# Performance work log

Hardware: AMD Instinct MI355X
Metric: run time of the kernel (lower is better)

## Reference

```python
import jax, jax.numpy as jnp
import numpy as np

D = 256
H = 4
HD = D // H


def setup_inputs() -> dict:
    key = jax.random.key(0)
    ks = jax.random.split(key, 12)
    A, T = 64, 512
    s = 1.0 / np.sqrt(D)
    return {
        "features": jax.random.normal(ks[0], (A, T, D), jnp.float32),
        "positions": jax.random.normal(ks[1], (A, T, 2), jnp.float32),
        "Wq": jax.random.normal(ks[2], (D, D), jnp.float32) * s,
        "bq": jnp.zeros((D,), jnp.float32),
        "Wk": jax.random.normal(ks[3], (D, D), jnp.float32) * s,
        "bk": jnp.zeros((D,), jnp.float32),
        "Wv": jax.random.normal(ks[4], (D, D), jnp.float32) * s,
        "bv": jnp.zeros((D,), jnp.float32),
        "Wo": jax.random.normal(ks[5], (D, D), jnp.float32) * s,
        "bo": jnp.zeros((D,), jnp.float32),
        "max_distance": 2,
        "time_window": 64,
    }


def _sparse_mask(positions, max_distance, time_window):
    # positions: [A, T, 2] -> allowed [A, T, T]
    A, T, _ = positions.shape
    diff = positions[:, :, None, :] - positions[:, None, :, :]  # [A,T,T,2]
    dist2 = jnp.sum(diff * diff, axis=-1)                       # [A,T,T]
    t = jnp.arange(T)
    tmask = jnp.abs(t[:, None] - t[None, :]) <= time_window      # [T,T]
    return (dist2 <= float(max_distance) ** 2) & tmask[None]     # [A,T,T]


def reference(features, positions, Wq, bq, Wk, bk, Wv, bv, Wo, bo,
              max_distance, time_window):
    A, T, Dm = features.shape
    allowed = _sparse_mask(positions, max_distance, time_window)  # [A,T,T]
    q = features @ Wq.T + bq
    k = features @ Wk.T + bk
    v = features @ Wv.T + bv
    # split heads: [A, T, H, HD]
    q = q.reshape(A, T, H, HD)
    k = k.reshape(A, T, H, HD)
    v = v.reshape(A, T, H, HD)
    scale = 1.0 / np.sqrt(HD)
    scores = jnp.einsum("athd,ashd->ahts", q, k) * scale          # [A,H,T,T]
    scores = jnp.where(allowed[:, None], scores, -jnp.inf)
    attn = jax.nn.softmax(scores, axis=-1)
    out = jnp.einsum("ahts,ashd->athd", attn, v).reshape(A, T, Dm)
    return out @ Wo.T + bo
```

## Files before the change

kernel.cpp:

```cpp
#include <hip/hip_runtime.h>
#include <hip/hip_bf16.h>
#include <cstdint>
#include <cstddef>

typedef __attribute__((ext_vector_type(8))) _Float16 half8;
typedef __attribute__((ext_vector_type(4))) float floatx4;

#define MFMA16(a, b, c) __builtin_amdgcn_mfma_f32_16x16x32_f16((a), (b), (c), 0, 0, 0)

#define GLOAD_LDS16(g, l)                                                     \
    __builtin_amdgcn_global_load_lds(                                         \
        (const __attribute__((address_space(1))) void*)(g),                   \
        (__attribute__((address_space(3))) void*)(l), 16, 0, 0)

#define NFEAT 8388608

__device__ __forceinline__ void stage_dma(
    const _Float16* __restrict__ src, _Float16* __restrict__ lds,
    int wid, int lane)
{
#pragma unroll
    for (int i = 0; i < 4; ++i) {
        int grp = wid * 4 + i;
        int row = grp * 8 + (lane >> 3);
        int sc  = (lane & 7) ^ (row & 7);
        GLOAD_LDS16(src + (size_t)row * 256 + sc * 8, lds + grp * 512);
    }
}

__device__ __forceinline__ void stage_f32_s(
    const float* __restrict__ src, _Float16* __restrict__ lds, int tid,
    int dst_stride)
{
#pragma unroll
    for (int i = 0; i < 4; ++i) {
        int g   = tid + 256 * i;
        int row = g >> 3, chd = g & 7;
        int chs = chd ^ (row & 7);
        const float* s = src + (size_t)row * 256 + chs * 8;
        float4 v0 = *(const float4*)s;
        float4 v1 = *(const float4*)(s + 4);
        half8 h = { (_Float16)v0.x, (_Float16)v0.y, (_Float16)v0.z, (_Float16)v0.w,
                    (_Float16)v1.x, (_Float16)v1.y, (_Float16)v1.z, (_Float16)v1.w };
        *(half8*)(&lds[row * dst_stride + chd * 8]) = h;
    }
}

__global__ __launch_bounds__(256) void qkv_fused(
    const float* __restrict__ feat,
    const float* __restrict__ Wq, const float* __restrict__ Wk,
    const float* __restrict__ Wv,
    const float* __restrict__ bq, const float* __restrict__ bk,
    const float* __restrict__ bv,
    _Float16* __restrict__ Qb, _Float16* __restrict__ Kb, _Float16* __restrict__ Vb)
{
    __shared__ _Float16 Xs[128 * 256];
    __shared__ _Float16 Ws[128 * 64];

    const int n   = blockIdx.x;
    const int idx = n >> 3;
    const int bm  = (n & 7) * 32 + (idx >> 1);
    const int bn  = idx & 1;

    const int tid  = threadIdx.x;
    const int lane = tid & 63, wid = tid >> 6;
    const int quad = lane >> 4, l16 = lane & 15;
    const int wm = wid & 1, wn = wid >> 1;

    const float* Xg = feat + (size_t)bm * 128 * 256;
#pragma unroll
    for (int slab = 0; slab < 4; ++slab)
        stage_f32_s(Xg + slab * 64, Xs + slab * 64, tid, 256);
    __syncthreads();

#pragma unroll 1
    for (int z = 0; z < 3; ++z) {
        const float* W    = (z == 0) ? Wq : (z == 1) ? Wk : Wv;
        const float* bias = (z == 0) ? bq : (z == 1) ? bk : bv;
        _Float16*    outp = (z == 0) ? Qb : (z == 1) ? Kb : Vb;
        const float* Wg = W + (size_t)bn * 128 * 256;

        floatx4 acc[4][4] = {};
#pragma unroll 1
        for (int ks = 0; ks < 4; ++ks) {
            stage_f32_s(Wg + ks * 64, Ws, tid, 64);
            __syncthreads();
#pragma unroll
            for (int kh = 0; kh < 2; ++kh) {
                half8 af[4], bf[4];
#pragma unroll
                for (int mi = 0; mi < 4; ++mi) {
                    int row = wm * 64 + mi * 16 + l16;
                    int cs  = (kh * 4 + quad) ^ (row & 7);
                    af[mi] = *(const half8*)(&Xs[row * 256 + ks * 64 + cs * 8]);
                }
#pragma unroll
                for (int ni = 0; ni < 4; ++ni) {
                    int row = wn * 64 + ni * 16 + l16;
                    int cs  = (kh * 4 + quad) ^ (row & 7);
                    bf[ni] = *(const half8*)(&Ws[row * 64 + cs * 8]);
                }
#pragma unroll
                for (int mi = 0; mi < 4; ++mi)
#pragma unroll
                    for (int ni = 0; ni < 4; ++ni)
                        acc[mi][ni] = MFMA16(af[mi], bf[ni], acc[mi][ni]);
            }
            __syncthreads();
        }

#pragma unroll
        for (int ni = 0; ni < 4; ++ni) {
            int col = bn * 128 + wn * 64 + ni * 16 + l16;
            float bv2 = bias[col];
#pragma unroll
            for (int mi = 0; mi < 4; ++mi)
#pragma unroll
                for (int r = 0; r < 4; ++r) {
                    int row = bm * 128 + wm * 64 + mi * 16 + quad * 4 + r;
                    outp[(size_t)row * 256 + col] = (_Float16)(acc[mi][ni][r] + bv2);
                }
        }
    }
}

__global__ __launch_bounds__(256) void out_gemm(
    const _Float16* __restrict__ attnH, const float* __restrict__ Wo,
    const float* __restrict__ bo, float* __restrict__ out)
{
    __shared__ _Float16 As[128 * 64];
    __shared__ _Float16 Bs[128 * 64];

    const int n   = blockIdx.x;
    const int idx = n >> 3;
    const int bm  = (n & 7) * 32 + (idx >> 1);
    const int bn  = idx & 1;

    const int tid  = threadIdx.x;
    const int lane = tid & 63, wid = tid >> 6;
    const int quad = lane >> 4, l16 = lane & 15;
    const int wm = wid & 1, wn = wid >> 1;

    floatx4 acc[4][4] = {};
    const float* Wg = Wo + (size_t)bn * 128 * 256;

    for (int k0 = 0; k0 < 256; k0 += 64) {
        stage_dma(attnH + (size_t)bm * 128 * 256 + k0, As, wid, lane);
        stage_f32_s(Wg + k0, Bs, tid, 64);
        __syncthreads();
#pragma unroll
        for (int kh = 0; kh < 2; ++kh) {
            half8 af[4], bf[4];
#pragma unroll
            for (int mi = 0; mi < 4; ++mi) {
                int row = wm * 64 + mi * 16 + l16;
                int cs  = (kh * 4 + quad) ^ (row & 7);
                af[mi] = *(const half8*)(&As[row * 64 + cs * 8]);
            }
#pragma unroll
            for (int ni = 0; ni < 4; ++ni) {
                int row = wn * 64 + ni * 16 + l16;
                int cs  = (kh * 4 + quad) ^ (row & 7);
                bf[ni] = *(const half8*)(&Bs[row * 64 + cs * 8]);
            }
#pragma unroll
            for (int mi = 0; mi < 4; ++mi)
#pragma unroll
                for (int ni = 0; ni < 4; ++ni)
                    acc[mi][ni] = MFMA16(af[mi], bf[ni], acc[mi][ni]);
        }
        __syncthreads();
    }

#pragma unroll
    for (int ni = 0; ni < 4; ++ni) {
        int col = bn * 128 + wn * 64 + ni * 16 + l16;
        float bv = bo[col];
#pragma unroll
        for (int mi = 0; mi < 4; ++mi)
#pragma unroll
            for (int r = 0; r < 4; ++r) {
                int row = bm * 128 + wm * 64 + mi * 16 + quad * 4 + r;
                out[(size_t)row * 256 + col] = acc[mi][ni][r] + bv;
            }
    }
}

__global__ __launch_bounds__(256) void attn_kernel(
    const _Float16* __restrict__ Qb, const _Float16* __restrict__ Kb,
    const _Float16* __restrict__ Vb, const float* __restrict__ positions,
    const int* __restrict__ mdp, const int* __restrict__ twp,
    _Float16* __restrict__ attnb)
{
    const int n   = blockIdx.x;
    const int idx = n >> 3;
    const int a   = (n & 7) * 8 + (idx >> 5);
    const int rem = idx & 31;
    const int qt  = rem >> 2, h = rem & 3;

    const int q0 = qt * 64;
    const int s_base = q0 - 64;
    const int tid = threadIdx.x, lane = tid & 63, wid = tid >> 6;
    const int quad = lane >> 4, l16 = lane & 15;

    __shared__ _Float16 KPs[192 * 64];
    __shared__ _Float16 Vt[64 * 192];

    const size_t abase = (size_t)a * 512;
    const int md = *mdp, tw = *twp;
    const float md2 = (float)(md * md);

    const size_t qrow = abase + q0 + wid * 16 + l16;
    half8 aq0 = *(const half8*)(Qb + qrow * 256 + h * 64 + quad * 8);
    half8 aq1 = *(const half8*)(Qb + qrow * 256 + h * 64 + 32 + quad * 8);
    float qpx[4], qpy[4];
    int trow[4];
#pragma unroll
    for (int r = 0; r < 4; ++r) {
        int m = wid * 16 + quad * 4 + r;
        trow[r] = q0 + m;
        float2 qp = *(const float2*)(positions + (abase + q0 + m) * 2);
        qpx[r] = qp.x;
        qpy[r] = qp.y;
    }

#pragma unroll
    for (int i = 0; i < 6; ++i) {
        int grp = wid * 6 + i;
        int si  = grp * 8 + (lane >> 3);
        int sc  = min(max(s_base + si, 0), 511);
        int ch  = (lane & 7) ^ (si & 7);
        GLOAD_LDS16(Kb + (abase + sc) * 256 + h * 64 + ch * 8, KPs + grp * 512);
    }
#pragma unroll
    for (int i = 0; i < 3; ++i) {
        int g   = tid + 256 * i;
        int si2 = (g % 96) * 2;
        int d0  = (g / 96) * 8;
        int sa  = min(max(s_base + si2, 0), 511);
        int sb  = min(max(s_base + si2 + 1, 0), 511);
        half8 v0 = *(const half8*)(Vb + (abase + sa) * 256 + h * 64 + d0);
        half8 v1 = *(const half8*)(Vb + (abase + sb) * 256 + h * 64 + d0);
        int c = si2 >> 3;
#pragma unroll
        for (int j = 0; j < 8; ++j) {
            int d  = d0 + j;
            int cs = (c & ~7) | ((c & 7) ^ (d & 7));
            union { _Float16 hh[2]; uint32_t u; } p;
            p.hh[0] = v0[j]; p.hh[1] = v1[j];
            *(uint32_t*)(&Vt[d * 192 + cs * 8 + (si2 & 7)]) = p.u;
        }
    }
    __syncthreads();

    floatx4 S[12];
#pragma unroll
    for (int j = 0; j < 12; ++j) {
        int si = j * 16 + l16;
        half8 bk0 = *(const half8*)(&KPs[si * 64 + ((quad) ^ (si & 7)) * 8]);
        half8 bk1 = *(const half8*)(&KPs[si * 64 + ((4 + quad) ^ (si & 7)) * 8]);
        floatx4 acc = {};
        acc = MFMA16(aq0, bk0, acc);
        acc = MFMA16(aq1, bk1, acc);
        int sr = s_base + si;
        int sc = min(max(sr, 0), 511);
        float2 kp = *(const float2*)(positions + (abase + sc) * 2);
        bool svalid = (sr >= 0) && (sr < 512);
#pragma unroll
        for (int r = 0; r < 4; ++r) {
            float dx = qpx[r] - kp.x, dy = qpy[r] - kp.y;
            float d2 = dx * dx + dy * dy;
            int dt = trow[r] - sr; dt = dt < 0 ? -dt : dt;
            bool ok = svalid && (d2 <= md2) && (dt <= tw);
            S[j][r] = ok ? acc[r] * 0.125f : -1e30f;
        }
    }

    float minv[4];
#pragma unroll
    for (int r = 0; r < 4; ++r) {
        float m = -1e30f;
#pragma unroll
        for (int j = 0; j < 12; ++j) m = fmaxf(m, S[j][r]);
        m = fmaxf(m, __shfl_xor(m, 1));
        m = fmaxf(m, __shfl_xor(m, 2));
        m = fmaxf(m, __shfl_xor(m, 4));
        m = fmaxf(m, __shfl_xor(m, 8));
        float l = 0.f;
#pragma unroll
        for (int j = 0; j < 12; ++j) {
            float p = __expf(S[j][r] - m);
            S[j][r] = p;
            l += p;
        }
        l += __shfl_xor(l, 1);
        l += __shfl_xor(l, 2);
        l += __shfl_xor(l, 4);
        l += __shfl_xor(l, 8);
        minv[r] = 1.0f / l;
    }

    __syncthreads();

    _Float16* Ps = KPs + wid * (16 * 192);
#pragma unroll
    for (int j = 0; j < 12; ++j)
#pragma unroll
        for (int r = 0; r < 4; ++r) {
            int row = quad * 4 + r;
            int col = j * 16 + l16;
            int ch  = (col >> 3) ^ (row & 7);
            Ps[row * 192 + ch * 8 + (col & 7)] = (_Float16)(S[j][r] * minv[r]);
        }

    half8 af[6];
#pragma unroll
    for (int k = 0; k < 6; ++k) {
        int ch = (k * 4 + quad) ^ (l16 & 7);
        af[k] = *(const half8*)(&Ps[l16 * 192 + ch * 8]);
    }
#pragma unroll
    for (int nn = 0; nn < 4; ++nn) {
        floatx4 accO = {};
#pragma unroll
        for (int k = 0; k < 6; ++k) {
            int row = nn * 16 + l16;
            int c   = k * 4 + quad;
            int cs  = (c & ~7) | ((c & 7) ^ (row & 7));
            half8 bv = *(const half8*)(&Vt[row * 192 + cs * 8]);
            accO = MFMA16(af[k], bv, accO);
        }
#pragma unroll
        for (int r = 0; r < 4; ++r) {
            int row = q0 + wid * 16 + quad * 4 + r;
            attnb[(abase + row) * 256 + h * 64 + nn * 16 + l16] = (_Float16)accO[r];
        }
    }
}

extern "C" void kernel_launch(void* const* d_in, const int* in_sizes, int n_in,
                              void* d_out, int out_size, void* d_ws, size_t ws_size,
                              hipStream_t stream)
{
    const float* feat = (const float*)d_in[0];
    const float* pos  = (const float*)d_in[1];
    const float* Wq   = (const float*)d_in[2];
    const float* bq   = (const float*)d_in[3];
    const float* Wk   = (const float*)d_in[4];
    const float* bk   = (const float*)d_in[5];
    const float* Wv   = (const float*)d_in[6];
    const float* bv   = (const float*)d_in[7];
    const float* Wo   = (const float*)d_in[8];
    const float* bo   = (const float*)d_in[9];
    const int*   md   = (const int*)d_in[10];
    const int*   tw   = (const int*)d_in[11];
    float*       out  = (float*)d_out;

    _Float16* ws    = (_Float16*)d_ws;
    _Float16* Qb    = ws;
    _Float16* Kb    = Qb + NFEAT;
    _Float16* Vb    = Kb + NFEAT;
    _Float16* attnH = Vb + NFEAT;

    qkv_fused<<<512, 256, 0, stream>>>(feat, Wq, Wk, Wv, bq, bk, bv, Qb, Kb, Vb);

    attn_kernel<<<2048, 256, 0, stream>>>(Qb, Kb, Vb, pos, md, tw, attnH);

    out_gemm<<<512, 256, 0, stream>>>(attnH, Wo, bo, out);
}
```

Measured before the change: 166.2 us.

## Prefetch weight tiles into registers and preload attention tile in projection GEMMs

In both the QKV projection and output projection GEMMs, the next fp32 weight k-slab is loaded into registers while the current slab is consumed. It is converted to fp16 and written to LDS at the start of the next step, replacing the previous synchronous stage-then-barrier loop. The QKV kernel also prefetches the first slab of the next weight matrix across z iterations. The output GEMM now DMA-loads the whole 128x256 attention tile into LDS up front instead of per k-step. The aim is to hide global load latency behind MFMA work, at the cost of more registers, more LDS and hand-written barrier/waitcnt asm.

```diff
diff --git a/kernel.cpp b/kernel.cpp
--- a/kernel.cpp
+++ b/kernel.cpp
@@ -13,20 +13,9 @@
         (const __attribute__((address_space(1))) void*)(g),                   \
         (__attribute__((address_space(3))) void*)(l), 16, 0, 0)
 
+#define BARLG() asm volatile("s_waitcnt lgkmcnt(0)\ns_barrier" ::: "memory")
+
 #define NFEAT 8388608
-
-__device__ __forceinline__ void stage_dma(
-    const _Float16* __restrict__ src, _Float16* __restrict__ lds,
-    int wid, int lane)
-{
-#pragma unroll
-    for (int i = 0; i < 4; ++i) {
-        int grp = wid * 4 + i;
-        int row = grp * 8 + (lane >> 3);
-        int sc  = (lane & 7) ^ (row & 7);
-        GLOAD_LDS16(src + (size_t)row * 256 + sc * 8, lds + grp * 512);
-    }
-}
 
 __device__ __forceinline__ void stage_f32_s(
     const float* __restrict__ src, _Float16* __restrict__ lds, int tid,
@@ -71,20 +60,49 @@
 #pragma unroll
     for (int slab = 0; slab < 4; ++slab)
         stage_f32_s(Xg + slab * 64, Xs + slab * 64, tid, 256);
+
+    float4 wv0[4], wv1[4];
+    auto loadw = [&](const float* __restrict__ src) {
+#pragma unroll
+        for (int i = 0; i < 4; ++i) {
+            int g = tid + 256 * i, row = g >> 3, chd = g & 7;
+            int chs = chd ^ (row & 7);
+            const float* s = src + (size_t)row * 256 + chs * 8;
+            wv0[i] = *(const float4*)s;
+            wv1[i] = *(const float4*)(s + 4);
+        }
+    };
+    auto writew = [&]() {
+#pragma unroll
+        for (int i = 0; i < 4; ++i) {
+            int g = tid + 256 * i, row = g >> 3, chd = g & 7;
+            half8 h = { (_Float16)wv0[i].x, (_Float16)wv0[i].y,
+                        (_Float16)wv0[i].z, (_Float16)wv0[i].w,
+                        (_Float16)wv1[i].x, (_Float16)wv1[i].y,
+                        (_Float16)wv1[i].z, (_Float16)wv1[i].w };
+            *(half8*)(&Ws[row * 64 + chd * 8]) = h;
+        }
+    };
+
+    const size_t boff = (size_t)bn * 128 * 256;
+    loadw(Wq + boff);
     __syncthreads();
 
 #pragma unroll 1
     for (int z = 0; z < 3; ++z) {
-        const float* W    = (z == 0) ? Wq : (z == 1) ? Wk : Wv;
+        const float* Wz   = (z == 0) ? Wq : (z == 1) ? Wk : Wv;
+        const float* Wnz  = (z == 0) ? Wk : Wv;
         const float* bias = (z == 0) ? bq : (z == 1) ? bk : bv;
         _Float16*    outp = (z == 0) ? Qb : (z == 1) ? Kb : Vb;
-        const float* Wg = W + (size_t)bn * 128 * 256;
 
         floatx4 acc[4][4] = {};
-#pragma unroll 1
+#pragma unroll
         for (int ks = 0; ks < 4; ++ks) {
-            stage_f32_s(Wg + ks * 64, Ws, tid, 64);
-            __syncthreads();
+            BARLG();
+            writew();
+            if (ks < 3)      loadw(Wz + boff + (ks + 1) * 64);
+            else if (z < 2)  loadw(Wnz + boff);
+            BARLG();
 #pragma unroll
             for (int kh = 0; kh < 2; ++kh) {
                 half8 af[4], bf[4];
@@ -106,7 +124,6 @@
                     for (int ni = 0; ni < 4; ++ni)
                         acc[mi][ni] = MFMA16(af[mi], bf[ni], acc[mi][ni]);
             }
-            __syncthreads();
         }
 
 #pragma unroll
@@ -128,7 +145,7 @@
     const _Float16* __restrict__ attnH, const float* __restrict__ Wo,
     const float* __restrict__ bo, float* __restrict__ out)
 {
-    __shared__ _Float16 As[128 * 64];
+    __shared__ _Float16 As[128 * 256];
     __shared__ _Float16 Bs[128 * 64];
 
     const int n   = blockIdx.x;
@@ -141,13 +158,51 @@
     const int quad = lane >> 4, l16 = lane & 15;
     const int wm = wid & 1, wn = wid >> 1;
 
+#pragma unroll
+    for (int slab = 0; slab < 4; ++slab)
+#pragma unroll
+        for (int i = 0; i < 4; ++i) {
+            int grp = wid * 4 + i;
+            int row = grp * 8 + (lane >> 3);
+            int sc  = (lane & 7) ^ (row & 7);
+            GLOAD_LDS16(attnH + (size_t)(bm * 128 + row) * 256 + slab * 64 + sc * 8,
+                        As + slab * 8192 + grp * 512);
+        }
+
+    float4 wv0[4], wv1[4];
+    auto loadw = [&](const float* __restrict__ src) {
+#pragma unroll
+        for (int i = 0; i < 4; ++i) {
+            int g = tid + 256 * i, row = g >> 3, chd = g & 7;
+            int chs = chd ^ (row & 7);
+            const float* s = src + (size_t)row * 256 + chs * 8;
+            wv0[i] = *(const float4*)s;
+            wv1[i] = *(const float4*)(s + 4);
+        }
+    };
+    auto writew = [&]() {
+#pragma unroll
+        for (int i = 0; i < 4; ++i) {
+            int g = tid + 256 * i, row = g >> 3, chd = g & 7;
+            half8 h = { (_Float16)wv0[i].x, (_Float16)wv0[i].y,
+                        (_Float16)wv0[i].z, (_Float16)wv0[i].w,
+                        (_Float16)wv1[i].x, (_Float16)wv1[i].y,
+                        (_Float16)wv1[i].z, (_Float16)wv1[i].w };
+            *(half8*)(&Bs[row * 64 + chd * 8]) = h;
+        }
+    };
+
+    const size_t boff = (size_t)bn * 128 * 256;
+    loadw(Wo + boff);
+    __syncthreads();
+
     floatx4 acc[4][4] = {};
-    const float* Wg = Wo + (size_t)bn * 128 * 256;
-
-    for (int k0 = 0; k0 < 256; k0 += 64) {
-        stage_dma(attnH + (size_t)bm * 128 * 256 + k0, As, wid, lane);
-        stage_f32_s(Wg + k0, Bs, tid, 64);
-        __syncthreads();
+#pragma unroll
+    for (int ks = 0; ks < 4; ++ks) {
+        BARLG();
+        writew();
+        if (ks < 3) loadw(Wo + boff + (ks + 1) * 64);
+        BARLG();
 #pragma unroll
         for (int kh = 0; kh < 2; ++kh) {
             half8 af[4], bf[4];
@@ -155,7 +210,7 @@
             for (int mi = 0; mi < 4; ++mi) {
                 int row = wm * 64 + mi * 16 + l16;
                 int cs  = (kh * 4 + quad) ^ (row & 7);
-                af[mi] = *(const half8*)(&As[row * 64 + cs * 8]);
+                af[mi] = *(const half8*)(&As[ks * 8192 + row * 64 + cs * 8]);
             }
 #pragma unroll
             for (int ni = 0; ni < 4; ++ni) {
@@ -169,7 +224,6 @@
                 for (int ni = 0; ni < 4; ++ni)
                     acc[mi][ni] = MFMA16(af[mi], bf[ni], acc[mi][ni]);
         }
-        __syncthreads();
     }
 
 #pragma unroll
```

Result: no change. 164.0 us, median of 2 (-1.3%).
